# Optimization experiments

Measured on AMD Instinct MI355X. Metric: run time of the kernel, lower is better.

Reference implementation:

```python
import jax, jax.numpy as jnp
import numpy as np

D_MODEL = 768
NUM_HEADS = 12
D_K = D_MODEL // NUM_HEADS
B, S = 8, 1024


def setup_inputs() -> dict:
    key = jax.random.key(0)
    ks = jax.random.split(key, 10)
    sc = 1.0 / np.sqrt(D_MODEL)
    inp = {
        'x': jax.random.normal(ks[0], (B, S, D_MODEL), dtype=jnp.float32),
        'mask': jnp.tril(jnp.ones((1, 1, S, S), dtype=jnp.int32)),
        'W_q': jax.random.normal(ks[1], (D_MODEL, D_MODEL), jnp.float32) * sc,
        'b_q': jnp.zeros((D_MODEL,), jnp.float32),
        'W_k': jax.random.normal(ks[2], (D_MODEL, D_MODEL), jnp.float32) * sc,
        'b_k': jnp.zeros((D_MODEL,), jnp.float32),
        'W_v': jax.random.normal(ks[3], (D_MODEL, D_MODEL), jnp.float32) * sc,
        'b_v': jnp.zeros((D_MODEL,), jnp.float32),
        'W_o': jax.random.normal(ks[4], (D_MODEL, D_MODEL), jnp.float32) * sc,
        'b_o': jnp.zeros((D_MODEL,), jnp.float32),
    }
    return inp


def reference(x, mask, W_q, b_q, W_k, b_k, W_v, b_v, W_o, b_o):
    b, s, d = x.shape
    # project (torch Linear: y = x @ W.T + b; here weights stored as [in, out])
    q = (x @ W_q + b_q).reshape(b, s, NUM_HEADS, D_K).transpose(0, 2, 1, 3)
    k = (x @ W_k + b_k).reshape(b, s, NUM_HEADS, D_K).transpose(0, 2, 1, 3)
    v = (x @ W_v + b_v).reshape(b, s, NUM_HEADS, D_K).transpose(0, 2, 1, 3)
    scores = jnp.einsum('bhqd,bhkd->bhqk', q, k) / jnp.sqrt(jnp.float32(D_K))
    scores = jnp.where(mask == 0, jnp.float32(-jnp.inf), scores)
    attn = jax.nn.softmax(scores, axis=-1)  # dropout: eval mode (identity)
    out = jnp.einsum('bhqk,bhkd->bhqd', attn, v)
    out = out.transpose(0, 2, 1, 3).reshape(b, s, d)
    return out @ W_o + b_o
```

## Files before the change

kernel.cpp:

```cpp
#include <hip/hip_runtime.h>
#include <hip/hip_bf16.h>
#include <stdint.h>

typedef __attribute__((ext_vector_type(8))) short short8;
typedef __attribute__((ext_vector_type(4))) short s16x4;
typedef __attribute__((ext_vector_type(4))) float f32x4;

#define GLDS16(gp, lp) __builtin_amdgcn_global_load_lds( \
    (const __attribute__((address_space(1))) void*)(gp), \
    (__attribute__((address_space(3))) void*)(lp), 16, 0, 0)

__device__ __forceinline__ unsigned short f2bf(float f) {
  union { float f; unsigned u; } v; v.f = f;
  unsigned r = v.u + 0x7FFFu + ((v.u >> 16) & 1u);
  return (unsigned short)(r >> 16);
}

__device__ __forceinline__ short bfpack(float f) {
  union { float f; unsigned u; } v; v.f = f;
  return (short)((v.u + 0x8000u) >> 16);
}

__global__ __launch_bounds__(256) void cast_x(const float* __restrict__ x,
                                              unsigned short* __restrict__ o, int n4) {
  int i = blockIdx.x * 256 + threadIdx.x;
  if (i < n4) {
    float4 v = ((const float4*)x)[i];
    union { unsigned short u[4]; unsigned long long ll; } r;
    r.u[0] = f2bf(v.x); r.u[1] = f2bf(v.y); r.u[2] = f2bf(v.z); r.u[3] = f2bf(v.w);
    ((unsigned long long*)o)[i] = r.ll;
  }
}

__global__ __launch_bounds__(256) void cast_wt4(const float* __restrict__ W0,
                                                const float* __restrict__ W1,
                                                const float* __restrict__ W2,
                                                const float* __restrict__ W3,
                                                unsigned short* __restrict__ T0,
                                                unsigned short* __restrict__ T1,
                                                unsigned short* __restrict__ T2,
                                                unsigned short* __restrict__ T3) {
  __shared__ float t[16][17];
  const int z = blockIdx.z;
  const float* W = z == 0 ? W0 : (z == 1 ? W1 : (z == 2 ? W2 : W3));
  unsigned short* Wt = z == 0 ? T0 : (z == 1 ? T1 : (z == 2 ? T2 : T3));
  int tx = threadIdx.x, ty = threadIdx.y;
  int c0 = blockIdx.x * 16, r0 = blockIdx.y * 16;
  t[ty][tx] = W[(size_t)(r0 + ty) * 768 + c0 + tx];
  __syncthreads();
  Wt[(size_t)(c0 + ty) * 768 + r0 + tx] = f2bf(t[tx][ty]);
}

__global__ __launch_bounds__(256) void trans_v(const unsigned short* __restrict__ Vb,
                                               unsigned short* __restrict__ Vt) {
  __shared__ unsigned short t[64][65];
  int b = blockIdx.z;
  int c0 = blockIdx.x * 64, s0 = blockIdx.y * 64;
  int tx = threadIdx.x & 63, ty = threadIdx.x >> 6;
  const unsigned short* src = Vb + (size_t)b * 1024 * 768;
  unsigned short* dst = Vt + (size_t)b * 768 * 1024;
#pragma unroll
  for (int i = 0; i < 16; ++i) {
    int s = ty + 4 * i;
    t[s][tx] = src[(size_t)(s0 + s) * 768 + c0 + tx];
  }
  __syncthreads();
  const int px = (tx & ~31) | (((tx >> 2) & 3) << 3) | (((tx >> 4) & 1) << 2) | (tx & 3);
#pragma unroll
  for (int i = 0; i < 16; ++i) {
    int c = ty + 4 * i;
    dst[(size_t)(c0 + c) * 1024 + s0 + px] = t[tx][c];
  }
}

__device__ __forceinline__ void gemm_core(const unsigned short* __restrict__ A,
                                          const unsigned short* __restrict__ Bt,
                                          int row0, int col0, f32x4 acc[4][4],
                                          unsigned short* sA, unsigned short* sB) {
  const int t = threadIdx.x, l = t & 63;
  const int w = t >> 6, wr = w >> 1, wc = w & 1;
  const int lr = l & 15, lk = l >> 4;
  const int rs = t >> 2;
  const int csw = ((t & 3) ^ (rs & 3) ^ ((t >> 4) & 3)) * 8;
  const int rsw = (lr & 3) ^ (lr >> 2);
  const unsigned short* Ar = A + (size_t)(row0 + rs) * 768 + csw;
  const unsigned short* Br = Bt + (size_t)(col0 + rs) * 768 + csw;

#define GSTAGE(BUF, K0)                                                     \
  do {                                                                      \
    GLDS16(Ar + (K0), sA + (BUF) * 4096 + t * 8);                           \
    GLDS16(Ar + (size_t)64 * 768 + (K0), sA + (BUF) * 4096 + 2048 + t * 8); \
    GLDS16(Br + (K0), sB + (BUF) * 4096 + t * 8);                           \
    GLDS16(Br + (size_t)64 * 768 + (K0), sB + (BUF) * 4096 + 2048 + t * 8); \
  } while (0)

  GSTAGE(0, 0);
#pragma unroll 1
  for (int kt = 0; kt < 24; ++kt) {
    __syncthreads();
    if (kt + 1 < 24) GSTAGE((kt + 1) & 1, (kt + 1) * 32);
    const unsigned short* cA = sA + (kt & 1) * 4096;
    const unsigned short* cB = sB + (kt & 1) * 4096;
    short8 af[4], bfr[4];
#pragma unroll
    for (int i = 0; i < 4; ++i)
      af[i] = *(const short8*)(cA + (wr * 64 + i * 16 + lr) * 32 + ((lk ^ rsw) * 8));
#pragma unroll
    for (int i = 0; i < 4; ++i)
      bfr[i] = *(const short8*)(cB + (wc * 64 + i * 16 + lr) * 32 + ((lk ^ rsw) * 8));
    __builtin_amdgcn_s_setprio(1);
#pragma unroll
    for (int i = 0; i < 4; ++i)
#pragma unroll
      for (int j = 0; j < 4; ++j)
        acc[i][j] = __builtin_amdgcn_mfma_f32_16x16x32_bf16(af[i], bfr[j], acc[i][j], 0, 0, 0);
    __builtin_amdgcn_s_setprio(0);
  }
#undef GSTAGE
}

__global__ __launch_bounds__(256, 3) void gemm_qkv(const unsigned short* __restrict__ A,
                                                   const unsigned short* __restrict__ Bt,
                                                   const float* __restrict__ bq,
                                                   const float* __restrict__ bk,
                                                   const float* __restrict__ bv,
                                                   unsigned short* __restrict__ Qb,
                                                   unsigned short* __restrict__ Kb,
                                                   unsigned short* __restrict__ Vb) {
  __shared__ unsigned short sA[2][128 * 32];
  __shared__ unsigned short sB[2][128 * 32];
  const int row0 = blockIdx.x * 128, col0 = blockIdx.y * 128;
  f32x4 acc[4][4] = {};
  gemm_core(A, Bt, row0, col0, acc, &sA[0][0], &sB[0][0]);

  const int l = threadIdx.x & 63, w = threadIdx.x >> 6;
  const int wr = w >> 1, wc = w & 1, lr = l & 15, lk = l >> 4;
  const int which = (blockIdx.y * 128) / 768;
  unsigned short* outp = which == 0 ? Qb : (which == 1 ? Kb : Vb);
  const float* bias = which == 0 ? bq : (which == 1 ? bk : bv);
  const float scale = which == 0 ? 0.18033688011112042f : 1.0f;
  const int ncb = col0 - which * 768;
#pragma unroll
  for (int i = 0; i < 4; ++i)
#pragma unroll
    for (int j = 0; j < 4; ++j) {
      int n = ncb + wc * 64 + j * 16 + lr;
      float bn = bias[n];
#pragma unroll
      for (int r = 0; r < 4; ++r) {
        int m = row0 + wr * 64 + i * 16 + lk * 4 + r;
        outp[(size_t)m * 768 + n] = f2bf((acc[i][j][r] + bn) * scale);
      }
    }
}

__global__ __launch_bounds__(256, 3) void gemm_out(const unsigned short* __restrict__ A,
                                                   const unsigned short* __restrict__ Bt,
                                                   const float* __restrict__ bias,
                                                   float* __restrict__ C) {
  __shared__ unsigned short sA[2][128 * 32];
  __shared__ unsigned short sB[2][128 * 32];
  const int row0 = blockIdx.x * 128, col0 = blockIdx.y * 128;
  f32x4 acc[4][4] = {};
  gemm_core(A, Bt, row0, col0, acc, &sA[0][0], &sB[0][0]);

  const int l = threadIdx.x & 63, w = threadIdx.x >> 6;
  const int wr = w >> 1, wc = w & 1, lr = l & 15, lk = l >> 4;
#pragma unroll
  for (int i = 0; i < 4; ++i)
#pragma unroll
    for (int j = 0; j < 4; ++j) {
      int n = col0 + wc * 64 + j * 16 + lr;
      float bn = bias[n];
#pragma unroll
      for (int r = 0; r < 4; ++r) {
        int m = row0 + wr * 64 + i * 16 + lk * 4 + r;
        C[(size_t)m * 768 + n] = acc[i][j][r] + bn;
      }
    }
}

__global__ __launch_bounds__(256, 3) void attn(const unsigned short* __restrict__ Q,
                                               const unsigned short* __restrict__ Kg,
                                               const unsigned short* __restrict__ V2,
                                               unsigned short* __restrict__ O) {
  __shared__ unsigned short Kl[2][4096];
  __shared__ unsigned short Vl[2][4096];
  const int tid = threadIdx.x;
  const int l = tid & 63, w = tid >> 6;
  const int lr = l & 15, lk = l >> 4;
  const int o = blockIdx.x;
  const int b = o & 7, rem = o >> 3, pair = rem & 7, h = rem >> 3;
  const int hd = h * 64;
  const size_t bS = (size_t)b * 1024;
  const unsigned short* Kbase = Kg + bS * 768 + hd;
  const unsigned short* Vbase = V2 + ((size_t)b * 768 + hd) * 1024;
  const int rs = tid >> 3;
  const int kcol = ((tid & 7) ^ (rs & 7)) * 8;
  const int swz = (lr & 7);
  const int qloc = w * 16 + lr;

#define STAGE(BUF, T)                                                          \
  do {                                                                         \
    const size_t kv0_ = (size_t)(T) * 64;                                      \
    GLDS16(Kbase + (kv0_ + rs) * 768 + kcol, &Kl[BUF][tid * 8]);               \
    GLDS16(Kbase + (kv0_ + rs + 32) * 768 + kcol, &Kl[BUF][(256 + tid) * 8]);  \
    GLDS16(Vbase + (size_t)rs * 1024 + kv0_ + kcol, &Vl[BUF][tid * 8]);        \
    GLDS16(Vbase + (size_t)(rs + 32) * 1024 + kv0_ + kcol,                     \
           &Vl[BUF][(256 + tid) * 8]);                                         \
  } while (0)

#pragma unroll 1
  for (int half = 0; half < 2; ++half) {
    const int qt = half ? 15 - pair : pair;
    const int qw = qt * 64 + w * 16;
    const int ntile = qt + 1;
    short8 bq0, bq1;
    {
      size_t qb = (bS + qw + lr) * 768 + hd + lk * 8;
      bq0 = *(const short8*)(Q + qb);
      bq1 = *(const short8*)(Q + qb + 32);
    }
    f32x4 oc0 = {}, oc1 = {}, oc2 = {}, oc3 = {};
    float lsum = 0.f;

    __syncthreads();
    STAGE(0, 0);

#pragma unroll 1
    for (int t = 0; t < ntile; ++t) {
      __syncthreads();
      if (t + 1 < ntile) STAGE((t + 1) & 1, t + 1);
      const unsigned short* Kb_ = Kl[t & 1];
      const unsigned short* Vb_ = Vl[t & 1];
      short8 kf00 = *(const short8*)(Kb_ + (0 * 16 + lr) * 64 + (((0 * 4 + lk) ^ swz) * 8));
      short8 kf01 = *(const short8*)(Kb_ + (0 * 16 + lr) * 64 + (((1 * 4 + lk) ^ swz) * 8));
      short8 kf10 = *(const short8*)(Kb_ + (1 * 16 + lr) * 64 + (((0 * 4 + lk) ^ swz) * 8));
      short8 kf11 = *(const short8*)(Kb_ + (1 * 16 + lr) * 64 + (((1 * 4 + lk) ^ swz) * 8));
      short8 kf20 = *(const short8*)(Kb_ + (2 * 16 + lr) * 64 + (((0 * 4 + lk) ^ swz) * 8));
      short8 kf21 = *(const short8*)(Kb_ + (2 * 16 + lr) * 64 + (((1 * 4 + lk) ^ swz) * 8));
      short8 kf30 = *(const short8*)(Kb_ + (3 * 16 + lr) * 64 + (((0 * 4 + lk) ^ swz) * 8));
      short8 kf31 = *(const short8*)(Kb_ + (3 * 16 + lr) * 64 + (((1 * 4 + lk) ^ swz) * 8));
      short8 vf00 = *(const short8*)(Vb_ + (0 * 16 + lr) * 64 + (((0 * 4 + lk) ^ swz) * 8));
      short8 vf01 = *(const short8*)(Vb_ + (0 * 16 + lr) * 64 + (((1 * 4 + lk) ^ swz) * 8));
      short8 vf10 = *(const short8*)(Vb_ + (1 * 16 + lr) * 64 + (((0 * 4 + lk) ^ swz) * 8));
      short8 vf11 = *(const short8*)(Vb_ + (1 * 16 + lr) * 64 + (((1 * 4 + lk) ^ swz) * 8));
      short8 vf20 = *(const short8*)(Vb_ + (2 * 16 + lr) * 64 + (((0 * 4 + lk) ^ swz) * 8));
      short8 vf21 = *(const short8*)(Vb_ + (2 * 16 + lr) * 64 + (((1 * 4 + lk) ^ swz) * 8));
      short8 vf30 = *(const short8*)(Vb_ + (3 * 16 + lr) * 64 + (((0 * 4 + lk) ^ swz) * 8));
      short8 vf31 = *(const short8*)(Vb_ + (3 * 16 + lr) * 64 + (((1 * 4 + lk) ^ swz) * 8));

      f32x4 s0 = {}, s1 = {}, s2 = {}, s3 = {};
      __builtin_amdgcn_s_setprio(1);
      s0 = __builtin_amdgcn_mfma_f32_16x16x32_bf16(kf00, bq0, s0, 0, 0, 0);
      s0 = __builtin_amdgcn_mfma_f32_16x16x32_bf16(kf01, bq1, s0, 0, 0, 0);
      s1 = __builtin_amdgcn_mfma_f32_16x16x32_bf16(kf10, bq0, s1, 0, 0, 0);
      s1 = __builtin_amdgcn_mfma_f32_16x16x32_bf16(kf11, bq1, s1, 0, 0, 0);
      s2 = __builtin_amdgcn_mfma_f32_16x16x32_bf16(kf20, bq0, s2, 0, 0, 0);
      s2 = __builtin_amdgcn_mfma_f32_16x16x32_bf16(kf21, bq1, s2, 0, 0, 0);
      s3 = __builtin_amdgcn_mfma_f32_16x16x32_bf16(kf30, bq0, s3, 0, 0, 0);
      s3 = __builtin_amdgcn_mfma_f32_16x16x32_bf16(kf31, bq1, s3, 0, 0, 0);
      __builtin_amdgcn_s_setprio(0);

      if (t == ntile - 1) {
        const int kb = lk * 4;
#pragma unroll
        for (int r = 0; r < 4; ++r) {
          if (kb + 0 + r > qloc) s0[r] = -1e30f;
          if (kb + 16 + r > qloc) s1[r] = -1e30f;
          if (kb + 32 + r > qloc) s2[r] = -1e30f;
          if (kb + 48 + r > qloc) s3[r] = -1e30f;
        }
      }
      float p0[4], p1[4], p2[4], p3[4];
#pragma unroll
      for (int r = 0; r < 4; ++r) {
        p0[r] = __builtin_amdgcn_exp2f(s0[r]);
        p1[r] = __builtin_amdgcn_exp2f(s1[r]);
        p2[r] = __builtin_amdgcn_exp2f(s2[r]);
        p3[r] = __builtin_amdgcn_exp2f(s3[r]);
      }
      lsum += ((p0[0] + p0[1]) + (p0[2] + p0[3])) + ((p1[0] + p1[1]) + (p1[2] + p1[3])) +
              ((p2[0] + p2[1]) + (p2[2] + p2[3])) + ((p3[0] + p3[1]) + (p3[2] + p3[3]));
      short8 pb0, pb1;
#pragma unroll
      for (int r = 0; r < 4; ++r) {
        pb0[r] = bfpack(p0[r]); pb0[r + 4] = bfpack(p1[r]);
        pb1[r] = bfpack(p2[r]); pb1[r + 4] = bfpack(p3[r]);
      }
      __builtin_amdgcn_s_setprio(1);
      oc0 = __builtin_amdgcn_mfma_f32_16x16x32_bf16(vf00, pb0, oc0, 0, 0, 0);
      oc0 = __builtin_amdgcn_mfma_f32_16x16x32_bf16(vf01, pb1, oc0, 0, 0, 0);
      oc1 = __builtin_amdgcn_mfma_f32_16x16x32_bf16(vf10, pb0, oc1, 0, 0, 0);
      oc1 = __builtin_amdgcn_mfma_f32_16x16x32_bf16(vf11, pb1, oc1, 0, 0, 0);
      oc2 = __builtin_amdgcn_mfma_f32_16x16x32_bf16(vf20, pb0, oc2, 0, 0, 0);
      oc2 = __builtin_amdgcn_mfma_f32_16x16x32_bf16(vf21, pb1, oc2, 0, 0, 0);
      oc3 = __builtin_amdgcn_mfma_f32_16x16x32_bf16(vf30, pb0, oc3, 0, 0, 0);
      oc3 = __builtin_amdgcn_mfma_f32_16x16x32_bf16(vf31, pb1, oc3, 0, 0, 0);
      __builtin_amdgcn_s_setprio(0);
    }

    lsum += __shfl_xor(lsum, 16);
    lsum += __shfl_xor(lsum, 32);
    const float inv = 1.f / lsum;
    unsigned short* op = O + (bS + qw + lr) * 768 + hd + lk * 4;
    s16x4 o0, o1, o2, o3;
#pragma unroll
    for (int r = 0; r < 4; ++r) {
      o0[r] = (short)f2bf(oc0[r] * inv);
      o1[r] = (short)f2bf(oc1[r] * inv);
      o2[r] = (short)f2bf(oc2[r] * inv);
      o3[r] = (short)f2bf(oc3[r] * inv);
    }
    *(s16x4*)(op) = o0;
    *(s16x4*)(op + 16) = o1;
    *(s16x4*)(op + 32) = o2;
    *(s16x4*)(op + 48) = o3;
  }
#undef STAGE
}

extern "C" void kernel_launch(void* const* d_in, const int* in_sizes, int n_in,
                              void* d_out, int out_size, void* d_ws, size_t ws_size,
                              hipStream_t stream) {
  const float* x  = (const float*)d_in[0];
  const float* Wq = (const float*)d_in[2]; const float* bq = (const float*)d_in[3];
  const float* Wk = (const float*)d_in[4]; const float* bk = (const float*)d_in[5];
  const float* Wv = (const float*)d_in[6]; const float* bv = (const float*)d_in[7];
  const float* Wo = (const float*)d_in[8]; const float* bo = (const float*)d_in[9];
  float* out = (float*)d_out;

  char* ws = (char*)d_ws;
  unsigned short* xb  = (unsigned short*)ws;
  unsigned short* WtQ = (unsigned short*)(ws + (size_t)12582912);
  unsigned short* WtK = WtQ + 589824;
  unsigned short* WtV = WtK + 589824;
  unsigned short* WtO = WtV + 589824;
  unsigned short* Qb  = (unsigned short*)(ws + (size_t)12582912 + (size_t)4 * 1179648);
  unsigned short* Kb  = Qb + 6291456;
  unsigned short* Vb  = Kb + 6291456;
  unsigned short* Vt  = Vb + 6291456;
  unsigned short* Ob  = xb;

  cast_x<<<6144, 256, 0, stream>>>(x, xb, 1572864);
  cast_wt4<<<dim3(48, 48, 4), dim3(16, 16), 0, stream>>>(Wq, Wk, Wv, Wo, WtQ, WtK, WtV, WtO);
  gemm_qkv<<<dim3(64, 18), 256, 0, stream>>>(xb, WtQ, bq, bk, bv, Qb, Kb, Vb);
  trans_v<<<dim3(12, 16, 8), 256, 0, stream>>>(Vb, Vt);
  attn<<<768, 256, 0, stream>>>(Qb, Kb, Vt, Ob);
  gemm_out<<<dim3(64, 6), 256, 0, stream>>>(Ob, WtO, bo, out);
}
```

Baseline: 113.6 us.

## Fuse V transpose into QKV GEMM epilogue and restructure GEMM prefetch pipeline

```diff
diff --git a/kernel.cpp b/kernel.cpp
--- a/kernel.cpp
+++ b/kernel.cpp
@@ -51,28 +51,6 @@
   Wt[(size_t)(c0 + ty) * 768 + r0 + tx] = f2bf(t[tx][ty]);
 }
 
-__global__ __launch_bounds__(256) void trans_v(const unsigned short* __restrict__ Vb,
-                                               unsigned short* __restrict__ Vt) {
-  __shared__ unsigned short t[64][65];
-  int b = blockIdx.z;
-  int c0 = blockIdx.x * 64, s0 = blockIdx.y * 64;
-  int tx = threadIdx.x & 63, ty = threadIdx.x >> 6;
-  const unsigned short* src = Vb + (size_t)b * 1024 * 768;
-  unsigned short* dst = Vt + (size_t)b * 768 * 1024;
-#pragma unroll
-  for (int i = 0; i < 16; ++i) {
-    int s = ty + 4 * i;
-    t[s][tx] = src[(size_t)(s0 + s) * 768 + c0 + tx];
-  }
-  __syncthreads();
-  const int px = (tx & ~31) | (((tx >> 2) & 3) << 3) | (((tx >> 4) & 1) << 2) | (tx & 3);
-#pragma unroll
-  for (int i = 0; i < 16; ++i) {
-    int c = ty + 4 * i;
-    dst[(size_t)(c0 + c) * 1024 + s0 + px] = t[tx][c];
-  }
-}
-
 __device__ __forceinline__ void gemm_core(const unsigned short* __restrict__ A,
                                           const unsigned short* __restrict__ Bt,
                                           int row0, int col0, f32x4 acc[4][4],
@@ -94,29 +72,45 @@
     GLDS16(Br + (size_t)64 * 768 + (K0), sB + (BUF) * 4096 + 2048 + t * 8); \
   } while (0)
 
+#define GCOMPUTE(PAR)                                                            \
+  do {                                                                           \
+    const unsigned short* cA = sA + (PAR) * 4096;                                \
+    const unsigned short* cB = sB + (PAR) * 4096;                                \
+    short8 af[4], bfr[4];                                                        \
+    _Pragma("unroll") for (int i = 0; i < 4; ++i)                                \
+        af[i] = *(const short8*)(cA + (wr * 64 + i * 16 + lr) * 32 + ((lk ^ rsw) * 8)); \
+    _Pragma("unroll") for (int i = 0; i < 4; ++i)                                \
+        bfr[i] = *(const short8*)(cB + (wc * 64 + i * 16 + lr) * 32 + ((lk ^ rsw) * 8)); \
+    __builtin_amdgcn_s_setprio(1);                                               \
+    _Pragma("unroll") for (int i = 0; i < 4; ++i)                                \
+        _Pragma("unroll") for (int j = 0; j < 4; ++j)                            \
+            acc[i][j] = __builtin_amdgcn_mfma_f32_16x16x32_bf16(af[i], bfr[j], acc[i][j], 0, 0, 0); \
+    __builtin_amdgcn_s_setprio(0);                                               \
+  } while (0)
+
   GSTAGE(0, 0);
+  GSTAGE(1, 32);
 #pragma unroll 1
-  for (int kt = 0; kt < 24; ++kt) {
-    __syncthreads();
-    if (kt + 1 < 24) GSTAGE((kt + 1) & 1, (kt + 1) * 32);
-    const unsigned short* cA = sA + (kt & 1) * 4096;
-    const unsigned short* cB = sB + (kt & 1) * 4096;
-    short8 af[4], bfr[4];
-#pragma unroll
-    for (int i = 0; i < 4; ++i)
-      af[i] = *(const short8*)(cA + (wr * 64 + i * 16 + lr) * 32 + ((lk ^ rsw) * 8));
-#pragma unroll
-    for (int i = 0; i < 4; ++i)
-      bfr[i] = *(const short8*)(cB + (wc * 64 + i * 16 + lr) * 32 + ((lk ^ rsw) * 8));
-    __builtin_amdgcn_s_setprio(1);
-#pragma unroll
-    for (int i = 0; i < 4; ++i)
-#pragma unroll
-      for (int j = 0; j < 4; ++j)
-        acc[i][j] = __builtin_amdgcn_mfma_f32_16x16x32_bf16(af[i], bfr[j], acc[i][j], 0, 0, 0);
-    __builtin_amdgcn_s_setprio(0);
+  for (int kt = 0; kt < 22; ++kt) {
+    asm volatile("s_waitcnt vmcnt(4)" ::: "memory");
+    __builtin_amdgcn_s_barrier();
+    __builtin_amdgcn_sched_barrier(0);
+    GCOMPUTE(kt & 1);
+    __builtin_amdgcn_sched_barrier(0);
+    __builtin_amdgcn_s_barrier();
+    __builtin_amdgcn_sched_barrier(0);
+    GSTAGE(kt & 1, (kt + 2) * 32);
   }
+  asm volatile("s_waitcnt vmcnt(4)" ::: "memory");
+  __builtin_amdgcn_s_barrier();
+  __builtin_amdgcn_sched_barrier(0);
+  GCOMPUTE(0);
+  asm volatile("s_waitcnt vmcnt(0)" ::: "memory");
+  __builtin_amdgcn_s_barrier();
+  __builtin_amdgcn_sched_barrier(0);
+  GCOMPUTE(1);
 #undef GSTAGE
+#undef GCOMPUTE
 }
 
 __global__ __launch_bounds__(256, 3) void gemm_qkv(const unsigned short* __restrict__ A,
@@ -126,7 +120,7 @@
                                                    const float* __restrict__ bv,
                                                    unsigned short* __restrict__ Qb,
                                                    unsigned short* __restrict__ Kb,
-                                                   unsigned short* __restrict__ Vb) {
+                                                   unsigned short* __restrict__ Vt) {
   __shared__ unsigned short sA[2][128 * 32];
   __shared__ unsigned short sB[2][128 * 32];
   const int row0 = blockIdx.x * 128, col0 = blockIdx.y * 128;
@@ -136,22 +130,40 @@
   const int l = threadIdx.x & 63, w = threadIdx.x >> 6;
   const int wr = w >> 1, wc = w & 1, lr = l & 15, lk = l >> 4;
   const int which = (blockIdx.y * 128) / 768;
-  unsigned short* outp = which == 0 ? Qb : (which == 1 ? Kb : Vb);
-  const float* bias = which == 0 ? bq : (which == 1 ? bk : bv);
-  const float scale = which == 0 ? 0.18033688011112042f : 1.0f;
   const int ncb = col0 - which * 768;
-#pragma unroll
-  for (int i = 0; i < 4; ++i)
-#pragma unroll
-    for (int j = 0; j < 4; ++j) {
-      int n = ncb + wc * 64 + j * 16 + lr;
-      float bn = bias[n];
-#pragma unroll
-      for (int r = 0; r < 4; ++r) {
-        int m = row0 + wr * 64 + i * 16 + lk * 4 + r;
-        outp[(size_t)m * 768 + n] = f2bf((acc[i][j][r] + bn) * scale);
-      }
-    }
+  if (which == 2) {
+    const int bb = row0 >> 10;
+    const int sb = (row0 & 1023) + wr * 64;
+#pragma unroll
+    for (int i = 0; i < 4; ++i) {
+      const int sp = sb + (i >> 1) * 32 + lk * 8 + (i & 1) * 4;
+#pragma unroll
+      for (int j = 0; j < 4; ++j) {
+        const int n = ncb + wc * 64 + j * 16 + lr;
+        const float bn = bv[n];
+        s16x4 vv;
+#pragma unroll
+        for (int r = 0; r < 4; ++r) vv[r] = (short)f2bf(acc[i][j][r] + bn);
+        *(s16x4*)(Vt + ((size_t)(bb * 768 + n)) * 1024 + sp) = vv;
+      }
+    }
+  } else {
+    unsigned short* outp = which == 0 ? Qb : Kb;
+    const float* bias = which == 0 ? bq : bk;
+    const float scale = which == 0 ? 0.18033688011112042f : 1.0f;
+#pragma unroll
+    for (int i = 0; i < 4; ++i)
+#pragma unroll
+      for (int j = 0; j < 4; ++j) {
+        int n = ncb + wc * 64 + j * 16 + lr;
+        float bn = bias[n];
+#pragma unroll
+        for (int r = 0; r < 4; ++r) {
+          int m = row0 + wr * 64 + i * 16 + lk * 4 + r;
+          outp[(size_t)m * 768 + n] = f2bf((acc[i][j][r] + bn) * scale);
+        }
+      }
+  }
 }
 
 __global__ __launch_bounds__(256, 3) void gemm_out(const unsigned short* __restrict__ A,
@@ -338,14 +350,12 @@
   unsigned short* WtO = WtV + 589824;
   unsigned short* Qb  = (unsigned short*)(ws + (size_t)12582912 + (size_t)4 * 1179648);
   unsigned short* Kb  = Qb + 6291456;
-  unsigned short* Vb  = Kb + 6291456;
-  unsigned short* Vt  = Vb + 6291456;
+  unsigned short* Vt  = Kb + 2 * 6291456;
   unsigned short* Ob  = xb;
 
   cast_x<<<6144, 256, 0, stream>>>(x, xb, 1572864);
   cast_wt4<<<dim3(48, 48, 4), dim3(16, 16), 0, stream>>>(Wq, Wk, Wv, Wo, WtQ, WtK, WtV, WtO);
-  gemm_qkv<<<dim3(64, 18), 256, 0, stream>>>(xb, WtQ, bq, bk, bv, Qb, Kb, Vb);
-  trans_v<<<dim3(12, 16, 8), 256, 0, stream>>>(Vb, Vt);
+  gemm_qkv<<<dim3(64, 18), 256, 0, stream>>>(xb, WtQ, bq, bk, bv, Qb, Kb, Vt);
   attn<<<768, 256, 0, stream>>>(Qb, Kb, Vt, Ob);
   gemm_out<<<dim3(64, 6), 256, 0, stream>>>(Ob, WtO, bo, out);
 }
```

New measurement: 107.3 us. 5.6% less time.
